# Kernel optimization log

Hardware: AMD Instinct MI355X
Metric: run time of the kernel (lower is better)

Reference implementation:

```python
import jax, jax.numpy as jnp
import numpy as np

H = 768
NH = 12
HD = H // NH  # 64


def setup_inputs() -> dict:
    key = jax.random.key(0)
    ks = jax.random.split(key, 10)
    B, S = 8, 1024
    x = jax.random.normal(ks[0], (B, S, H), dtype=jnp.float32)
    attention_mask = jax.random.randint(ks[1], (B, S), 0, 2, dtype=jnp.int32)
    s = 1.0 / np.sqrt(H)
    Wq = jax.random.normal(ks[2], (H, H), jnp.float32) * s
    bq = jnp.zeros((H,), jnp.float32)
    Wk = jax.random.normal(ks[3], (H, H), jnp.float32) * s
    bk = jnp.zeros((H,), jnp.float32)
    Wv = jax.random.normal(ks[4], (H, H), jnp.float32) * s
    bv = jnp.zeros((H,), jnp.float32)
    Wo = jax.random.normal(ks[5], (H, H), jnp.float32) * s
    bo = jnp.zeros((H,), jnp.float32)
    return {"x": x, "attention_mask": attention_mask,
            "Wq": Wq, "bq": bq, "Wk": Wk, "bk": bk,
            "Wv": Wv, "bv": bv, "Wo": Wo, "bo": bo}


def reference(x, attention_mask, Wq, bq, Wk, bk, Wv, bv, Wo, bo):
    B, S, _ = x.shape
    scale = HD ** -0.5
    # projections -> [B, NH, S, HD]
    def split_heads(t):
        return t.reshape(B, S, NH, HD).transpose(0, 2, 1, 3)
    q = split_heads(x @ Wq.T + bq)
    k = split_heads(x @ Wk.T + bk)
    v = split_heads(x @ Wv.T + bv)
    scores = jnp.einsum('bhqd,bhkd->bhqk', q, k) * scale  # [B,NH,S,S]
    mask = attention_mask[:, None, None, :]  # [B,1,1,S]
    scores = jnp.where(mask == 0, jnp.float32(-10000.0), scores)
    probs = jax.nn.softmax(scores, axis=-1)
    ctx = jnp.einsum('bhqk,bhkd->bhqd', probs, v)  # [B,NH,S,HD]
    ctx = ctx.transpose(0, 2, 1, 3).reshape(B, S, H)
    out = ctx @ Wo.T + bo
    return out
```

## Files before the change

### kernel.cpp

```cpp
#include <hip/hip_runtime.h>
#include <hip/hip_bf16.h>

#define HDIM 768
#define NH 12
#define HD 64
#define BB 8
#define SS 1024
#define MROWS (BB*SS)
#define NQKV (3*HDIM)

#define SCL2E 0.18033688011f
#define MASKNEG -14426.9504f

typedef __attribute__((ext_vector_type(8))) short bf16x8;
typedef __attribute__((ext_vector_type(4))) float f32x4;

__device__ __forceinline__ unsigned short f2bf(float f) {
    unsigned int u = __float_as_uint(f);
    unsigned int r = (u + 0x7fffu + ((u >> 16) & 1u)) >> 16;
    return (unsigned short)r;
}

__device__ __forceinline__ void gload_lds16(const void* gsrc, void* ldst) {
    __builtin_amdgcn_global_load_lds(
        (const __attribute__((address_space(1))) unsigned int*)gsrc,
        (__attribute__((address_space(3))) unsigned int*)ldst,
        16, 0, 0);
}

__global__ void pack_all(const float* __restrict__ x,
                         const float* __restrict__ Wq, const float* __restrict__ Wk,
                         const float* __restrict__ Wv, const float* __restrict__ Wo,
                         const float* __restrict__ bq, const float* __restrict__ bk,
                         const float* __restrict__ bv, const int* __restrict__ m,
                         unsigned short* __restrict__ xb, unsigned short* __restrict__ wqkv,
                         unsigned short* __restrict__ wo,
                         float* __restrict__ biasq, float* __restrict__ madd)
{
    const int tid = blockIdx.x * blockDim.x + threadIdx.x;
    const int stride = gridDim.x * blockDim.x;
    for (int i = tid; i < 2162688; i += stride) {
        const float* src; unsigned short* dst; int off;
        if (i < 1572864) { src = x; dst = xb; off = i; }
        else {
            int j = i - 1572864;
            int seg = j / 147456;
            off = j - seg * 147456;
            src = (seg == 0) ? Wq : (seg == 1) ? Wk : (seg == 2) ? Wv : Wo;
            dst = (seg == 3) ? wo : wqkv + seg * (HDIM * HDIM);
        }
        float4 v = reinterpret_cast<const float4*>(src)[off];
        union { unsigned short u[4]; unsigned long long q; } o;
        o.u[0] = f2bf(v.x); o.u[1] = f2bf(v.y); o.u[2] = f2bf(v.z); o.u[3] = f2bf(v.w);
        reinterpret_cast<unsigned long long*>(dst)[off] = o.q;
    }
    if (tid < 3 * HDIM)
        biasq[tid] = (tid < HDIM) ? bq[tid] : (tid < 2 * HDIM) ? bk[tid - HDIM] : bv[tid - 2 * HDIM];
    if (tid < BB * SS)
        madd[tid] = (m[tid] == 0) ? MASKNEG : 0.0f;
}

template<int MODE>
__global__ __launch_bounds__(256)
void gemm_bt(const unsigned short* __restrict__ A,
             const unsigned short* __restrict__ Bw,
             const float* __restrict__ bias,
             unsigned short* __restrict__ qb,
             unsigned short* __restrict__ kb,
             unsigned short* __restrict__ vtb,
             float* __restrict__ fout,
             int K, int gridN)
{
    __shared__ unsigned short As[2][128 * 32];
    __shared__ unsigned short Bs[2][128 * 32];
    const int tid  = threadIdx.x;
    const int wave = tid >> 6;
    const int lane = tid & 63;

    const int nwg = gridDim.x;
    const int cpx = nwg >> 3;
    const int wg  = (blockIdx.x & 7) * cpx + (blockIdx.x >> 3);
    const int bm = (wg / gridN) * 128;
    const int bn = (wg % gridN) * 128;

    const int wm = (wave >> 1) * 64;
    const int wn = (wave & 1) * 64;
    const int lr  = lane & 15;
    const int hv  = lane >> 4;
    const int sA  = (lr >> 1) & 3;
    const int srow4 = lane >> 2;
    const int sg4   = lane & 3;

    f32x4 zero4 = {0.f, 0.f, 0.f, 0.f};
    f32x4 acc[4][4];
#pragma unroll
    for (int i = 0; i < 4; i++)
#pragma unroll
        for (int j = 0; j < 4; j++) acc[i][j] = zero4;

    auto stage = [&](int buf, int k0) {
#pragma unroll
        for (int jj = 0; jj < 2; ++jj) {
            int rbase = wave * 32 + jj * 16;
            int r = rbase + srow4;
            int gk = (sg4 ^ ((r >> 1) & 3)) * 8;
            gload_lds16(A  + (size_t)(bm + r) * K + k0 + gk, &As[buf][rbase * 32]);
            gload_lds16(Bw + (size_t)(bn + r) * K + k0 + gk, &Bs[buf][rbase * 32]);
        }
    };

    stage(0, 0);
    if (K > 32) stage(1, 32);

    int buf = 0;
    for (int k0 = 0; k0 < K; k0 += 32) {
        if (k0 + 32 < K) { asm volatile("s_waitcnt vmcnt(4)" ::: "memory"); }
        else             { asm volatile("s_waitcnt vmcnt(0)" ::: "memory"); }
        __builtin_amdgcn_s_barrier();
        __builtin_amdgcn_sched_barrier(0);

        bf16x8 af[4], bf[4];
#pragma unroll
        for (int mi = 0; mi < 4; mi++)
            af[mi] = *(const bf16x8*)&As[buf][(wm + mi * 16 + lr) * 32 + ((hv ^ sA) * 8)];
#pragma unroll
        for (int ni = 0; ni < 4; ni++)
            bf[ni] = *(const bf16x8*)&Bs[buf][(wn + ni * 16 + lr) * 32 + ((hv ^ sA) * 8)];

#pragma unroll
        for (int mi = 0; mi < 4; mi++)
#pragma unroll
            for (int ni = 0; ni < 4; ni++)
                acc[mi][ni] = __builtin_amdgcn_mfma_f32_16x16x32_bf16(
                    af[mi], bf[ni], acc[mi][ni], 0, 0, 0);

        __builtin_amdgcn_s_barrier();
        if (k0 + 64 < K) stage(buf, k0 + 64);
        buf ^= 1;
    }

    const int rgrp = lane >> 4;
#pragma unroll
    for (int mi = 0; mi < 4; mi++)
#pragma unroll
        for (int ni = 0; ni < 4; ni++)
#pragma unroll
            for (int r = 0; r < 4; r++) {
                int m = bm + wm + mi * 16 + rgrp * 4 + r;
                int n = bn + wn + ni * 16 + lr;
                float v = acc[mi][ni][r] + bias[n];
                if (MODE == 0) {
                    int which = n / HDIM;
                    int nn = n - which * HDIM;
                    int h = nn >> 6, d = nn & 63;
                    int b = m >> 10, s = m & 1023;
                    unsigned short bvv = f2bf(v);
                    if (which == 0)      qb [(((size_t)(b * NH + h)) * SS + s) * HD + d] = bvv;
                    else if (which == 1) kb [(((size_t)(b * NH + h)) * SS + s) * HD + d] = bvv;
                    else                 vtb[(((size_t)(b * NH + h)) * HD + d) * SS + s] = bvv;
                } else {
                    fout[(size_t)m * HDIM + n] = v;
                }
            }
}

__global__ __launch_bounds__(256, 4)
void attn_kernel(const unsigned short* __restrict__ qb,
                 const unsigned short* __restrict__ kb,
                 const unsigned short* __restrict__ vtb,
                 const float* __restrict__ maskadd,
                 unsigned short* __restrict__ ctx)
{
    __shared__ unsigned short Ks[64][64];
    __shared__ unsigned short Vs[64][64];
    __shared__ unsigned short Ps[4][16][64];

    const int tid  = threadIdx.x;
    const int wave = tid >> 6;
    const int lane = tid & 63;
    const int wg = (blockIdx.x & 7) * 192 + (blockIdx.x >> 3);
    const int qt = wg & 15;
    const int h  = (wg >> 4) % NH;
    const int b  = wg / 192;
    const int bh = b * NH + h;
    const int q0 = qt * 64 + wave * 16;
    const int lr  = lane & 15;
    const int hi  = lane >> 4;
    const int e3  = lr & 7;
    const int srow = lane >> 3;
    const int sg   = lane & 7;

    const unsigned short* Qp = qb  + (size_t)bh * SS * HD;
    const unsigned short* Kp = kb  + (size_t)bh * SS * HD;
    const unsigned short* Vp = vtb + (size_t)bh * HD * SS;
    const float* madd = maskadd + b * SS;

    bf16x8 aq[2];
#pragma unroll
    for (int kk = 0; kk < 2; kk++)
        aq[kk] = *(const bf16x8*)&Qp[(size_t)(q0 + lr) * HD + kk * 32 + hi * 8];

    f32x4 zero4 = {0.f, 0.f, 0.f, 0.f};
    f32x4 o[4];
#pragma unroll
    for (int i = 0; i < 4; i++) o[i] = zero4;
    float plsum = 0.f;

    bf16x8 kreg[2], vreg[2];
    auto ld = [&](int t0) {
#pragma unroll
        for (int jj = 0; jj < 2; ++jj) {
            int rr = (wave * 2 + jj) * 8 + srow;
            kreg[jj] = *(const bf16x8*)&Kp[(size_t)(t0 + rr) * HD + sg * 8];
            vreg[jj] = *(const bf16x8*)&Vp[(size_t)rr * SS + t0 + sg * 8];
        }
    };
    auto wr = [&]() {
        const int slot = (sg ^ srow) * 8;
#pragma unroll
        for (int jj = 0; jj < 2; ++jj) {
            int rr = (wave * 2 + jj) * 8 + srow;
            *(bf16x8*)&Ks[rr][slot] = kreg[jj];
            *(bf16x8*)&Vs[rr][slot] = vreg[jj];
        }
    };

    ld(0);
    wr();
    __syncthreads();

    for (int t0 = 0; t0 < SS; t0 += 64) {
        const bool more = (t0 + 64 < SS);
        if (more) ld(t0 + 64);

        f32x4 sacc[4];
#pragma unroll
        for (int ni = 0; ni < 4; ni++) sacc[ni] = zero4;
        __builtin_amdgcn_s_setprio(1);
#pragma unroll
        for (int kk = 0; kk < 2; kk++)
#pragma unroll
            for (int ni = 0; ni < 4; ni++) {
                bf16x8 kf = *(const bf16x8*)&Ks[ni * 16 + lr][((kk * 4 + hi) ^ e3) * 8];
                sacc[ni] = __builtin_amdgcn_mfma_f32_16x16x32_bf16(kf, aq[kk], sacc[ni], 0, 0, 0);
            }
        __builtin_amdgcn_s_setprio(0);

        float4 md[4];
#pragma unroll
        for (int ni = 0; ni < 4; ni++)
            md[ni] = *(const float4*)&madd[t0 + ni * 16 + hi * 4];

        float p[4][4];
#pragma unroll
        for (int ni = 0; ni < 4; ni++) {
            p[ni][0] = __builtin_amdgcn_exp2f(fmaf(sacc[ni][0], SCL2E, md[ni].x));
            p[ni][1] = __builtin_amdgcn_exp2f(fmaf(sacc[ni][1], SCL2E, md[ni].y));
            p[ni][2] = __builtin_amdgcn_exp2f(fmaf(sacc[ni][2], SCL2E, md[ni].z));
            p[ni][3] = __builtin_amdgcn_exp2f(fmaf(sacc[ni][3], SCL2E, md[ni].w));
            plsum += p[ni][0] + p[ni][1] + p[ni][2] + p[ni][3];
        }

#pragma unroll
        for (int ni = 0; ni < 4; ni++) {
            union { __hip_bfloat162 h2[2]; unsigned long long q; } u;
            u.h2[0] = __float22bfloat162_rn(make_float2(p[ni][0], p[ni][1]));
            u.h2[1] = __float22bfloat162_rn(make_float2(p[ni][2], p[ni][3]));
            *(unsigned long long*)&Ps[wave][lr][((4 * ni + hi) ^ (e3 << 1)) * 4] = u.q;
        }

        __builtin_amdgcn_s_setprio(1);
#pragma unroll
        for (int ks = 0; ks < 2; ks++) {
            bf16x8 pa = *(const bf16x8*)&Ps[wave][lr][((8 * ks + 2 * hi) ^ (e3 << 1)) * 4];
#pragma unroll
            for (int nd = 0; nd < 4; nd++) {
                bf16x8 vb = *(const bf16x8*)&Vs[nd * 16 + lr][((4 * ks + hi) ^ e3) * 8];
                o[nd] = __builtin_amdgcn_mfma_f32_16x16x32_bf16(pa, vb, o[nd], 0, 0, 0);
            }
        }
        __builtin_amdgcn_s_setprio(0);

        __syncthreads();
        if (more) {
            wr();
            __syncthreads();
        }
    }

    float lrun = plsum;
    lrun += __shfl_xor(lrun, 16);
    lrun += __shfl_xor(lrun, 32);
    float iv[4];
#pragma unroll
    for (int r = 0; r < 4; r++) iv[r] = 1.0f / __shfl(lrun, hi * 4 + r, 16);
#pragma unroll
    for (int r = 0; r < 4; r++) {
        int grow = b * SS + qt * 64 + wave * 16 + hi * 4 + r;
#pragma unroll
        for (int nd = 0; nd < 4; nd++)
            ctx[(size_t)grow * HDIM + h * HD + nd * 16 + lr] = f2bf(o[nd][r] * iv[r]);
    }
}

extern "C" void kernel_launch(void* const* d_in, const int* in_sizes, int n_in,
                              void* d_out, int out_size, void* d_ws, size_t ws_size,
                              hipStream_t stream)
{
    const float* x    = (const float*)d_in[0];
    const int*   amask= (const int*)d_in[1];
    const float* Wq   = (const float*)d_in[2];
    const float* bq   = (const float*)d_in[3];
    const float* Wk   = (const float*)d_in[4];
    const float* bk   = (const float*)d_in[5];
    const float* Wv   = (const float*)d_in[6];
    const float* bv   = (const float*)d_in[7];
    const float* Wo   = (const float*)d_in[8];
    const float* bo   = (const float*)d_in[9];
    float* out = (float*)d_out;

    char* ws = (char*)d_ws;
    unsigned short* xb   = (unsigned short*)(ws);
    unsigned short* wqkv = (unsigned short*)(ws + 12582912);
    unsigned short* wo   = (unsigned short*)(ws + 16121856);
    float*          biasq= (float*)(ws + 17301504);
    unsigned short* qb   = (unsigned short*)(ws + 17310720);
    unsigned short* kb   = (unsigned short*)(ws + 29893632);
    unsigned short* vtb  = (unsigned short*)(ws + 42476544);
    unsigned short* ctx  = (unsigned short*)(ws + 55059456);
    float*          madd = (float*)(ws + 67642368);

    pack_all<<<2048, 256, 0, stream>>>(x, Wq, Wk, Wv, Wo, bq, bk, bv, amask,
                                       xb, wqkv, wo, biasq, madd);

    gemm_bt<0><<<(MROWS / 128) * (NQKV / 128), 256, 0, stream>>>(
        xb, wqkv, biasq, qb, kb, vtb, nullptr, HDIM, NQKV / 128);

    attn_kernel<<<(SS / 64) * NH * BB, 256, 0, stream>>>(qb, kb, vtb, madd, ctx);

    gemm_bt<1><<<(MROWS / 128) * (HDIM / 128), 256, 0, stream>>>(
        ctx, wo, bo, nullptr, nullptr, nullptr, out, HDIM, HDIM / 128);
}
```

Before: 148.4 us.

## Deepen GEMM LDS pipeline to four stages with single barrier per k-step

Changes the bf16 GEMM's LDS staging from double buffering to a 4-slot ring with three tiles prefetched ahead. The second barrier per iteration is removed by issuing the next stage right after the top barrier, and K is fixed at compile time so the loop fully unrolls. MFMA blocks are wrapped in s_setprio to favour the compute waves. LDS use doubles to 64KB per block, which may lower occupancy.

```diff
diff --git a/kernel.cpp b/kernel.cpp
--- a/kernel.cpp
+++ b/kernel.cpp
@@ -8,6 +8,8 @@
 #define SS 1024
 #define MROWS (BB*SS)
 #define NQKV (3*HDIM)
+#define GK 768
+#define NHALF (GK/32)
 
 #define SCL2E 0.18033688011f
 #define MASKNEG -14426.9504f
@@ -69,10 +71,10 @@
              unsigned short* __restrict__ kb,
              unsigned short* __restrict__ vtb,
              float* __restrict__ fout,
-             int K, int gridN)
+             int gridN)
 {
-    __shared__ unsigned short As[2][128 * 32];
-    __shared__ unsigned short Bs[2][128 * 32];
+    __shared__ unsigned short As[4][128 * 32];
+    __shared__ unsigned short Bs[4][128 * 32];
     const int tid  = threadIdx.x;
     const int wave = tid >> 6;
     const int lane = tid & 63;
@@ -87,9 +89,10 @@
     const int wn = (wave & 1) * 64;
     const int lr  = lane & 15;
     const int hv  = lane >> 4;
-    const int sA  = (lr >> 1) & 3;
-    const int srow4 = lane >> 2;
-    const int sg4   = lane & 3;
+    const int rsw = (lr >> 1) & 3;
+    const int srow = lane >> 2;
+    const int sslot = lane & 3;
+    const int skg = sslot ^ ((srow >> 1) & 3);
 
     f32x4 zero4 = {0.f, 0.f, 0.f, 0.f};
     f32x4 acc[4][4];
@@ -98,45 +101,48 @@
 #pragma unroll
         for (int j = 0; j < 4; j++) acc[i][j] = zero4;
 
-    auto stage = [&](int buf, int k0) {
-#pragma unroll
-        for (int jj = 0; jj < 2; ++jj) {
-            int rbase = wave * 32 + jj * 16;
-            int r = rbase + srow4;
-            int gk = (sg4 ^ ((r >> 1) & 3)) * 8;
-            gload_lds16(A  + (size_t)(bm + r) * K + k0 + gk, &As[buf][rbase * 32]);
-            gload_lds16(Bw + (size_t)(bn + r) * K + k0 + gk, &Bs[buf][rbase * 32]);
+    auto stage = [&](int h) {
+        const int slot = h & 3;
+        const int k0 = h * 32;
+#pragma unroll
+        for (int j = 0; j < 2; ++j) {
+            int rbase = (wave * 2 + j) * 16;
+            int row = rbase + srow;
+            gload_lds16(A  + (size_t)(bm + row) * GK + k0 + skg * 8, &As[slot][rbase * 32]);
+            gload_lds16(Bw + (size_t)(bn + row) * GK + k0 + skg * 8, &Bs[slot][rbase * 32]);
         }
     };
 
-    stage(0, 0);
-    if (K > 32) stage(1, 32);
-
-    int buf = 0;
-    for (int k0 = 0; k0 < K; k0 += 32) {
-        if (k0 + 32 < K) { asm volatile("s_waitcnt vmcnt(4)" ::: "memory"); }
-        else             { asm volatile("s_waitcnt vmcnt(0)" ::: "memory"); }
+    stage(0); stage(1); stage(2);
+
+#pragma unroll
+    for (int h = 0; h < NHALF; ++h) {
+        const int rem = NHALF - 1 - h;
+        if (rem >= 2)      { asm volatile("s_waitcnt vmcnt(8)" ::: "memory"); }
+        else if (rem == 1) { asm volatile("s_waitcnt vmcnt(4)" ::: "memory"); }
+        else               { asm volatile("s_waitcnt vmcnt(0)" ::: "memory"); }
         __builtin_amdgcn_s_barrier();
         __builtin_amdgcn_sched_barrier(0);
 
+        if (h + 3 < NHALF) stage(h + 3);
+
+        const int slot = h & 3;
         bf16x8 af[4], bf[4];
 #pragma unroll
         for (int mi = 0; mi < 4; mi++)
-            af[mi] = *(const bf16x8*)&As[buf][(wm + mi * 16 + lr) * 32 + ((hv ^ sA) * 8)];
+            af[mi] = *(const bf16x8*)&As[slot][(wm + mi * 16 + lr) * 32 + ((hv ^ rsw) * 8)];
 #pragma unroll
         for (int ni = 0; ni < 4; ni++)
-            bf[ni] = *(const bf16x8*)&Bs[buf][(wn + ni * 16 + lr) * 32 + ((hv ^ sA) * 8)];
-
+            bf[ni] = *(const bf16x8*)&Bs[slot][(wn + ni * 16 + lr) * 32 + ((hv ^ rsw) * 8)];
+
+        __builtin_amdgcn_s_setprio(1);
 #pragma unroll
         for (int mi = 0; mi < 4; mi++)
 #pragma unroll
             for (int ni = 0; ni < 4; ni++)
                 acc[mi][ni] = __builtin_amdgcn_mfma_f32_16x16x32_bf16(
                     af[mi], bf[ni], acc[mi][ni], 0, 0, 0);
-
-        __builtin_amdgcn_s_barrier();
-        if (k0 + 64 < K) stage(buf, k0 + 64);
-        buf ^= 1;
+        __builtin_amdgcn_s_setprio(0);
     }
 
     const int rgrp = lane >> 4;
@@ -334,10 +340,10 @@
                                        xb, wqkv, wo, biasq, madd);
 
     gemm_bt<0><<<(MROWS / 128) * (NQKV / 128), 256, 0, stream>>>(
-        xb, wqkv, biasq, qb, kb, vtb, nullptr, HDIM, NQKV / 128);
+        xb, wqkv, biasq, qb, kb, vtb, nullptr, NQKV / 128);
 
     attn_kernel<<<(SS / 64) * NH * BB, 256, 0, stream>>>(qb, kb, vtb, madd, ctx);
 
     gemm_bt<1><<<(MROWS / 128) * (HDIM / 128), 256, 0, stream>>>(
-        ctx, wo, bo, nullptr, nullptr, nullptr, out, HDIM, HDIM / 128);
-}
+        ctx, wo, bo, nullptr, nullptr, nullptr, out, HDIM / 128);
+}
```

Measured after the change: 147.1 us. No clear change (-0.9%).
